# Performance work log

Measured on AMD Instinct MI355X. Metric: run time of the kernel, lower is better.

The kernel has to match this reference:

```python
import jax, jax.numpy as jnp
import numpy as np

# ---- static ragged feature layout (from CTGAN metadata) ----
NUM_CLUSTERS = [10, 8, 10, 5, 10, 10, 7, 10, 10, 10]          # per numerical feature
NUM_CATEGORIES = [2, 5, 10, 3, 50, 4, 2, 8, 100, 6, 2, 3, 12, 5, 2, 30, 4, 9, 2, 7]
TAU = 0.2        # GumbelSoftmax temperature (teras default)
BN_EPS = 1e-3    # keras BatchNormalization default epsilon
LATENT_DIM = 128
BATCH = 65536

_seg, _alpha = [], []
_gid = 0
for c in NUM_CLUSTERS:
    _seg.append(_gid); _alpha.append(True); _gid += 1        # alpha scalar (tanh), own segment
    _seg += [_gid] * c; _alpha += [False] * c; _gid += 1     # beta cluster group (gumbel softmax)
for k in NUM_CATEGORIES:
    _seg += [_gid] * k; _alpha += [False] * k; _gid += 1     # categorical group (gumbel softmax)
SEG = jnp.asarray(np.array(_seg, dtype=np.int32))
ALPHA_MASK = jnp.asarray(np.array(_alpha, dtype=bool))
N_SEG = _gid
DATA_DIM = len(_seg)  # 366


def setup_inputs() -> dict:
    key = jax.random.key(0)
    ks = jax.random.split(key, 8)
    z = jax.random.normal(ks[0], (BATCH, LATENT_DIM), dtype=jnp.float32)
    # pre-sampled standard Gumbel noise for the gumbel-softmax groups
    u = jax.random.uniform(ks[1], (BATCH, DATA_DIM), dtype=jnp.float32, minval=1e-6, maxval=1.0 - 1e-6)
    g = -jnp.log(-jnp.log(u))
    def w(k, fi, fo):
        return jax.random.normal(k, (fi, fo), dtype=jnp.float32) * (1.0 / np.sqrt(fi))
    return {
        "z": z, "g": g,
        "W1": w(ks[2], LATENT_DIM, 256), "b1": jnp.zeros((256,), jnp.float32),
        "gamma1": jnp.ones((256,), jnp.float32), "beta1": jnp.zeros((256,), jnp.float32),
        "W2": w(ks[3], LATENT_DIM + 256, 256), "b2": jnp.zeros((256,), jnp.float32),
        "gamma2": jnp.ones((256,), jnp.float32), "beta2": jnp.zeros((256,), jnp.float32),
        "Wout": w(ks[4], LATENT_DIM + 512, DATA_DIM), "bout": jnp.zeros((DATA_DIM,), jnp.float32),
    }


def _bn_relu(h, gamma, beta):
    # training-mode batch norm (batch statistics), as used while training CTGAN
    mu = jnp.mean(h, axis=0)
    var = jnp.var(h, axis=0)
    return jax.nn.relu((h - mu) * jax.lax.rsqrt(var + BN_EPS) * gamma + beta)


def reference(z, g, W1, b1, gamma1, beta1, W2, b2, gamma2, beta2, Wout, bout):
    # CTGAN residual generator layers: out = concat([relu(bn(dense(x))), x])
    h1 = jnp.concatenate([_bn_relu(z @ W1 + b1, gamma1, beta1), z], axis=1)    # [B, 384]
    h2 = jnp.concatenate([_bn_relu(h1 @ W2 + b2, gamma2, beta2), h1], axis=1)  # [B, 640]
    logits = h2 @ Wout + bout                                                  # [B, 366]

    # ragged per-group gumbel-softmax: segment-wise stable softmax over columns
    zt = ((logits + g) / TAU).T                                   # [D, B]
    m = jax.ops.segment_max(zt, SEG, num_segments=N_SEG)          # [S, B]
    e = jnp.exp(zt - m[SEG])
    s = jax.ops.segment_sum(e, SEG, num_segments=N_SEG)
    soft = (e / s[SEG]).T                                         # [B, D]
    # alpha columns: tanh of raw logits; all other columns: group softmax
    return jnp.where(ALPHA_MASK[None, :], jnp.tanh(logits), soft)
```

## Files before the change

kernel.cpp:

```cpp
#include <hip/hip_runtime.h>

typedef _Float16 half_t;
typedef _Float16 half4 __attribute__((ext_vector_type(4)));
typedef _Float16 half8 __attribute__((ext_vector_type(8)));
typedef float f32x4 __attribute__((ext_vector_type(4)));

#define AS1 __attribute__((address_space(1)))
#define AS3 __attribute__((address_space(3)))

static constexpr int NBATCH = 65536;

__device__ __forceinline__ bool is_alpha(int c) {
  const unsigned long long AM0 =
      (1ull << 0) | (1ull << 11) | (1ull << 20) | (1ull << 31) | (1ull << 37) |
      (1ull << 48) | (1ull << 59);
  const unsigned long long AM1 = (1ull << 3) | (1ull << 14) | (1ull << 25);
  if (c >= 90) return false;
  return (((c < 64) ? (AM0 >> c) : (AM1 >> (c - 64))) & 1ull) != 0ull;
}

__device__ __forceinline__ half8 bn8(half8 x, half8 sc, half8 sh, half8 lo) {
  return __builtin_elementwise_max(x * sc + sh, lo);
}

__global__ __launch_bounds__(256) void k_prep(
    const float* __restrict__ z, half_t* __restrict__ zdst,
    const float* __restrict__ W1, half_t* __restrict__ W1t,
    const float* __restrict__ W2, half_t* __restrict__ W2t,
    const float* __restrict__ Wout, half_t* __restrict__ Wot,
    half_t* __restrict__ t2sc, half_t* __restrict__ t2sh, half_t* __restrict__ t2lo,
    half_t* __restrict__ t3sc, half_t* __restrict__ t3sh, half_t* __restrict__ t3lo) {
  const int b = blockIdx.x;
  const int tid = threadIdx.x;
  if (b < 4096) {
    size_t i = (size_t)b * 256 + tid;
    int row = (int)(i >> 4), c8 = (int)(i & 15) << 3;
    const float* s = z + (size_t)row * 128 + c8;
    float4 v0 = *(const float4*)s;
    float4 v1 = *(const float4*)(s + 4);
    half8 h;
    h[0]=(half_t)v0.x; h[1]=(half_t)v0.y; h[2]=(half_t)v0.z; h[3]=(half_t)v0.w;
    h[4]=(half_t)v1.x; h[5]=(half_t)v1.y; h[6]=(half_t)v1.z; h[7]=(half_t)v1.w;
    *(half8*)(zdst + (size_t)row * 640 + c8) = h;
  } else if (b < 4224) {
    int i = (b - 4096) * 256 + tid;
    int n = i >> 7, k = i & 127;
    W1t[i] = (half_t)W1[k * 256 + n];
  } else if (b < 4608) {
    int i = (b - 4224) * 256 + tid;
    int n = i / 384, k = i - n * 384;
    W2t[i] = (half_t)W2[k * 256 + n];
  } else if (b < 5568) {
    int i = (b - 4608) * 256 + tid;
    int n = i / 640, k = i - n * 640;
    Wot[i] = (half_t)((n < 366) ? Wout[k * 366 + n] : 0.f);
  } else {
    if (tid < 128) {
      t2sc[256 + tid] = (half_t)1.f; t2sh[256 + tid] = (half_t)0.f;
      t2lo[256 + tid] = (half_t)(-65504.f);
    } else {
      int t = tid - 128;
      t3sc[512 + t] = (half_t)1.f; t3sh[512 + t] = (half_t)0.f;
      t3lo[512 + t] = (half_t)(-65504.f);
    }
  }
}

template<bool STATS, bool TRANS, bool ALPHA>
__global__ __launch_bounds__(256) void k_gemm(
    const half_t* __restrict__ A, int lda, int K,
    const half_t* __restrict__ Bt,
    const float* __restrict__ bias,
    const half_t* __restrict__ tsc, const half_t* __restrict__ tsh,
    const half_t* __restrict__ tlo,
    half_t* __restrict__ o16, int ldo, int ncreal,
    float* __restrict__ ps, float* __restrict__ pq) {
  __shared__ __align__(16) char smem[32768];
  const int tid  = threadIdx.x;
  const int lane = tid & 63;
  const int w    = tid >> 6;
  const int wr   = w >> 1, wc = w & 1;
  const int ml   = lane & 15, g = lane >> 4;
  const int brow = blockIdx.x * 128;
  const int bcol = blockIdx.y * 128;
  const int sr  = lane >> 3;
  const int scg = (lane & 7) ^ sr;

  f32x4 acc[4][4];
#pragma unroll
  for (int i = 0; i < 4; i++)
#pragma unroll
    for (int j = 0; j < 4; j++) acc[i][j] = (f32x4){0.f, 0.f, 0.f, 0.f};

  const half_t* Abase = A  + (size_t)brow * lda;
  const half_t* Bbase = Bt + (size_t)bcol * K;
  const int nt = K >> 6;

  half_t* As = (half_t*)smem;
  half_t* Bs = (half_t*)(smem + 16384);

  for (int t = 0; t < nt; t++) {
    const int k0 = t * 64;
    half8 sc0, sh0, lo0, sc1, sh1, lo1;
    if (TRANS) {
      const int ka = k0 + g * 8, kb = k0 + 32 + g * 8;
      sc0 = *(const half8*)&tsc[ka]; sh0 = *(const half8*)&tsh[ka]; lo0 = *(const half8*)&tlo[ka];
      sc1 = *(const half8*)&tsc[kb]; sh1 = *(const half8*)&tsh[kb]; lo1 = *(const half8*)&tlo[kb];
    }
    if (t) __syncthreads();
#pragma unroll
    for (int it = 0; it < 4; it++) {
      int q = it * 4 + w;
      int r = q * 8 + sr;
      __builtin_amdgcn_global_load_lds(
          (AS1 const void*)(Abase + (size_t)r * lda + k0 + scg * 8),
          (AS3 void*)(As + q * 512), 16, 0, 0);
      __builtin_amdgcn_global_load_lds(
          (AS1 const void*)(Bbase + (size_t)r * K + k0 + scg * 8),
          (AS3 void*)(Bs + q * 512), 16, 0, 0);
    }
    __syncthreads();
#pragma unroll
    for (int t2 = 0; t2 < 2; t2++) {
      const int c4 = t2 * 4 + g;
      half8 af[4], bf[4];
#pragma unroll
      for (int fm = 0; fm < 4; fm++) {
        int row = wr * 64 + fm * 16 + ml;
        af[fm] = *(const half8*)((const char*)As + row * 128 + ((c4 ^ (row & 7)) << 4));
      }
      if (TRANS) {
        const half8 sc = t2 ? sc1 : sc0;
        const half8 sh = t2 ? sh1 : sh0;
        const half8 lo = t2 ? lo1 : lo0;
#pragma unroll
        for (int fm = 0; fm < 4; fm++) af[fm] = bn8(af[fm], sc, sh, lo);
      }
#pragma unroll
      for (int fn = 0; fn < 4; fn++) {
        int row = wc * 64 + fn * 16 + ml;
        bf[fn] = *(const half8*)((const char*)Bs + row * 128 + ((c4 ^ (row & 7)) << 4));
      }
#pragma unroll
      for (int fm = 0; fm < 4; fm++)
#pragma unroll
        for (int fn = 0; fn < 4; fn++)
          acc[fm][fn] = __builtin_amdgcn_mfma_f32_16x16x32_f16(af[fm], bf[fn], acc[fm][fn], 0, 0, 0);
    }
  }
  __syncthreads();

#pragma unroll
  for (int fn = 0; fn < 4; fn++) {
    int col  = wc * 64 + fn * 16 + ml;
    int gcol = bcol + col;
    float bz = (gcol < ncreal) ? bias[gcol] : 0.f;
    float s = 0.f, q = 0.f;
    const bool al = ALPHA && (gcol < 90) && is_alpha(gcol);
#pragma unroll
    for (int fm = 0; fm < 4; fm++)
#pragma unroll
      for (int rr = 0; rr < 4; rr++) {
        float v = acc[fm][fn][rr] + bz;
        if (STATS) { s += v; q += v * v; }
        if (al) v = tanhf(v);
        acc[fm][fn][rr] = v;
      }
    if (STATS) {
      s += __shfl_xor(s, 16, 64); s += __shfl_xor(s, 32, 64);
      q += __shfl_xor(q, 16, 64); q += __shfl_xor(q, 32, 64);
      if (g == 0) {
        ps[(size_t)gcol * 1024 + blockIdx.x * 2 + wr] = s;
        pq[(size_t)gcol * 1024 + blockIdx.x * 2 + wr] = q;
      }
    }
  }

  half_t* so = (half_t*)smem;
#pragma unroll
  for (int fn = 0; fn < 4; fn++)
#pragma unroll
    for (int fm = 0; fm < 4; fm++)
#pragma unroll
      for (int rr = 0; rr < 4; rr++)
        so[(wr * 64 + fm * 16 + g * 4 + rr) * 128 + wc * 64 + fn * 16 + ml] =
            (half_t)acc[fm][fn][rr];
  __syncthreads();
#pragma unroll
  for (int it = 0; it < 8; it++) {
    int r = it * 16 + (tid >> 4);
    int c = (tid & 15) * 8;
    *(half8*)(o16 + (size_t)(brow + r) * ldo + bcol + c) = *(const half8*)&so[r * 128 + c];
  }
}

__global__ __launch_bounds__(256) void k_bnfinal(
    const float* __restrict__ ps, const float* __restrict__ pq,
    const float* __restrict__ gamma, const float* __restrict__ beta,
    half_t* __restrict__ scA, half_t* __restrict__ shA, half_t* __restrict__ loA,
    half_t* __restrict__ scB, half_t* __restrict__ shB, half_t* __restrict__ loB) {
  int c = blockIdx.x, t = threadIdx.x;
  float s = 0.f, q = 0.f;
#pragma unroll
  for (int i = 0; i < 4; i++) {
    s += ps[(size_t)c * 1024 + t + i * 256];
    q += pq[(size_t)c * 1024 + t + i * 256];
  }
#pragma unroll
  for (int o = 1; o < 64; o <<= 1) { s += __shfl_xor(s, o, 64); q += __shfl_xor(q, o, 64); }
  __shared__ float ss[4], qq[4];
  if ((t & 63) == 0) { ss[t >> 6] = s; qq[t >> 6] = q; }
  __syncthreads();
  if (t == 0) {
    s = ss[0] + ss[1] + ss[2] + ss[3];
    q = qq[0] + qq[1] + qq[2] + qq[3];
    float mu   = s * (1.f / NBATCH);
    float var  = fmaxf(q * (1.f / NBATCH) - mu * mu, 0.f);
    float rstd = rsqrtf(var + 1e-3f);
    float a  = gamma[c] * rstd;
    float sh = beta[c] - mu * a;
    scA[c] = (half_t)a; shA[c] = (half_t)sh; loA[c] = (half_t)0.f;
    if (scB) { scB[c] = (half_t)a; shB[c] = (half_t)sh; loB[c] = (half_t)0.f; }
  }
}

template<int L>
__device__ __forceinline__ void seg_norm(float* __restrict__ zr, int S, int Lr) {
  float v[L];
#pragma unroll
  for (int j = 0; j < L; j++) v[j] = (j < Lr) ? zr[S + j] : -1e30f;
  float m = -1e30f;
#pragma unroll
  for (int j = 0; j < L; j++) m = fmaxf(m, v[j]);
  float s = 0.f;
#pragma unroll
  for (int j = 0; j < L; j++) { float e = __expf(v[j] - m); v[j] = e; s += e; }
  const float inv = 1.0f / s;
#pragma unroll
  for (int j = 0; j < L; j++)
    if (j < Lr) zr[S + j] = v[j] * inv;
}

template<int H>
__device__ __forceinline__ void seg_quad(float* __restrict__ zr, int base, int n) {
  float v[H];
#pragma unroll
  for (int j = 0; j < H; j++) v[j] = (j < n) ? zr[base + j] : -1e30f;
  float m = -1e30f;
#pragma unroll
  for (int j = 0; j < H; j++) m = fmaxf(m, v[j]);
  m = fmaxf(m, __shfl_xor(m, 1, 64));
  m = fmaxf(m, __shfl_xor(m, 2, 64));
  float s = 0.f;
#pragma unroll
  for (int j = 0; j < H; j++) { float e = __expf(v[j] - m); v[j] = e; s += e; }
  s += __shfl_xor(s, 1, 64);
  s += __shfl_xor(s, 2, 64);
  const float inv = 1.0f / s;
#pragma unroll
  for (int j = 0; j < H; j++)
    if (j < n) zr[base + j] = v[j] * inv;
}

__global__ __launch_bounds__(256, 6) void k_softmax(const half_t* __restrict__ lg,
                                                    const float* __restrict__ g,
                                                    float* __restrict__ out) {
  __shared__ float zb[16][373];
  const int tid  = threadIdx.x;
  const int row0 = blockIdx.x * 16;
  const size_t gbase = (size_t)row0 * 366;
  for (int i2 = tid; i2 < 16 * 183; i2 += 256) {
    int e0 = i2 * 2;
    int r = e0 / 366;
    int c = e0 - r * 366;
    const half_t* lp = lg + (size_t)(row0 + r) * 384 + c;
    float lx = (float)lp[0], ly = (float)lp[1];
    float2 gg = *(const float2*)(g + gbase + e0);
    zb[r][c]     = is_alpha(c)     ? lx : (lx + gg.x) * 5.0f;
    zb[r][c + 1] = is_alpha(c + 1) ? ly : (ly + gg.y) * 5.0f;
  }
  __syncthreads();
  {
    const int lane = tid & 63;
    const int w    = tid >> 6;
    const int quad = lane & 3;
    float* zr = &zb[lane >> 2][0];
    switch (w) {
      case 0:
        seg_quad<25>(zr, 184 + quad * 25, 25);
        break;
      case 1:
        seg_quad<13>(zr, 120 + quad * 13 - (quad >> 1) * (quad & 1), 13 - (quad >> 1));
        seg_quad<8>(zr, 314 + quad * 8 - (quad >> 1) * (quad & 1), 8 - (quad >> 1));
        break;
      case 2: {
        int s0 = (quad == 0) ? 295 : (quad == 1) ? 107 : (quad == 2) ? 38 : 68;
        int l0 = (quad == 0) ? 12 : 10;
        int s1 = (quad == 0) ? 1 : (quad == 1) ? 21 : (quad == 2) ? 49 : 79;
        int s2 = (quad == 0) ? 0 : (quad == 1) ? 100 : (quad == 2) ? 174 : 290;
        int l2 = (quad == 0) ? 0 : 2;
        seg_norm<12>(zr, s0, l0);
        seg_norm<10>(zr, s1, 10);
        seg_norm<2>(zr, s2, l2);
        break;
      }
      default: {
        int s0 = (quad == 0) ? 90 : (quad == 1) ? 12 : (quad == 2) ? 60 : 102;
        int l0 = (quad == 0) ? 10 : (quad == 1) ? 8 : (quad == 2) ? 7 : 5;
        int s1 = (quad == 0) ? 348 : (quad == 1) ? 176 : (quad == 2) ? 359 : 307;
        int l1 = (quad == 0) ? 9 : (quad == 1) ? 8 : (quad == 2) ? 7 : 5;
        int s2 = (quad == 0) ? 312 : (quad == 1) ? 284 : (quad == 2) ? 32 : 170;
        int l2 = (quad == 0) ? 2 : (quad == 1) ? 6 : (quad == 2) ? 5 : 4;
        int s3 = (quad == 0) ? 117 : (quad == 1) ? 357 : (quad == 2) ? 292 : 344;
        int l3 = (quad == 0) ? 3 : (quad == 1) ? 2 : (quad == 2) ? 3 : 4;
        seg_norm<10>(zr, s0, l0);
        seg_norm<9>(zr, s1, l1);
        seg_norm<6>(zr, s2, l2);
        seg_norm<4>(zr, s3, l3);
        break;
      }
    }
  }
  __syncthreads();
  for (int i2 = tid; i2 < 16 * 183; i2 += 256) {
    int e0 = i2 * 2;
    int r = e0 / 366;
    int c = e0 - r * 366;
    float2 v;
    v.x = zb[r][c];
    v.y = zb[r][c + 1];
    *(float2*)(out + gbase + e0) = v;
  }
}

extern "C" void kernel_launch(void* const* d_in, const int* in_sizes, int n_in,
                              void* d_out, int out_size, void* d_ws, size_t ws_size,
                              hipStream_t stream) {
  const float* z      = (const float*)d_in[0];
  const float* g      = (const float*)d_in[1];
  const float* W1     = (const float*)d_in[2];
  const float* b1     = (const float*)d_in[3];
  const float* gamma1 = (const float*)d_in[4];
  const float* beta1  = (const float*)d_in[5];
  const float* W2     = (const float*)d_in[6];
  const float* b2     = (const float*)d_in[7];
  const float* gamma2 = (const float*)d_in[8];
  const float* beta2  = (const float*)d_in[9];
  const float* Wout   = (const float*)d_in[10];
  const float* bout   = (const float*)d_in[11];
  float* out = (float*)d_out;
  char* ws = (char*)d_ws;

  size_t off = 0;
  half_t* act = (half_t*)(ws + off); off += (size_t)NBATCH * 640 * 2;
  half_t* lg  = (half_t*)(ws + off); off += (size_t)NBATCH * 384 * 2;
  half_t* W1t = (half_t*)(ws + off); off += (size_t)256 * 128 * 2;
  half_t* W2t = (half_t*)(ws + off); off += (size_t)256 * 384 * 2;
  half_t* Wot = (half_t*)(ws + off); off += (size_t)384 * 640 * 2;
  float*  ps  = (float*)(ws + off);  off += (size_t)256 * 1024 * 4;
  float*  pq  = (float*)(ws + off);  off += (size_t)256 * 1024 * 4;
  half_t* t2sc = (half_t*)(ws + off); off += 1024;
  half_t* t2sh = (half_t*)(ws + off); off += 1024;
  half_t* t2lo = (half_t*)(ws + off); off += 1024;
  half_t* t3sc = (half_t*)(ws + off); off += 2048;
  half_t* t3sh = (half_t*)(ws + off); off += 2048;
  half_t* t3lo = (half_t*)(ws + off); off += 2048;
  (void)ws_size; (void)in_sizes; (void)n_in; (void)out_size;

  k_prep<<<5569, 256, 0, stream>>>(z, act + 512, W1, W1t, W2, W2t, Wout, Wot,
                                   t2sc, t2sh, t2lo, t3sc, t3sh, t3lo);

  k_gemm<true, false, false><<<dim3(512, 2), 256, 0, stream>>>(
      act + 512, 640, 128, W1t, b1, nullptr, nullptr, nullptr,
      act + 256, 640, 256, ps, pq);
  k_bnfinal<<<256, 256, 0, stream>>>(ps, pq, gamma1, beta1,
                                     t2sc, t2sh, t2lo, t3sc + 256, t3sh + 256, t3lo + 256);

  k_gemm<true, true, false><<<dim3(512, 2), 256, 0, stream>>>(
      act + 256, 640, 384, W2t, b2, t2sc, t2sh, t2lo,
      act + 0, 640, 256, ps, pq);
  k_bnfinal<<<256, 256, 0, stream>>>(ps, pq, gamma2, beta2,
                                     t3sc, t3sh, t3lo, nullptr, nullptr, nullptr);

  k_gemm<false, true, true><<<dim3(512, 3), 256, 0, stream>>>(
      act, 640, 640, Wot, bout, t3sc, t3sh, t3lo,
      lg, 384, 366, nullptr, nullptr);

  k_softmax<<<NBATCH / 16, 256, 0, stream>>>(lg, g, out);
}
```

Baseline: 176.3 us.

## Triple-buffer GEMM K-loop with async global-to-LDS prefetch two tiles ahead

The GEMM main loop moves from a single-buffered 64-wide K tile, with two barriers per tile, to a 32-wide K tile held in a three-stage LDS ring. Loads for tile t+2 are issued before computing tile t, and raw s_waitcnt vmcnt plus a single s_barrier per step replace the double sync. The batch-norm scale, shift and clamp vectors are staged into LDS once at kernel start instead of being read from global memory every tile. In exchange, LDS use grows to 52 KB, which may reduce the number of resident blocks, and correctness depends on the hand-chosen vmcnt counts.

Result: no change. 178.1 us (+1.0%).

```diff
diff --git a/kernel.cpp b/kernel.cpp
--- a/kernel.cpp
+++ b/kernel.cpp
@@ -75,7 +75,7 @@
     const half_t* __restrict__ tlo,
     half_t* __restrict__ o16, int ldo, int ncreal,
     float* __restrict__ ps, float* __restrict__ pq) {
-  __shared__ __align__(16) char smem[32768];
+  __shared__ __align__(16) char smem[53248];
   const int tid  = threadIdx.x;
   const int lane = tid & 63;
   const int w    = tid >> 6;
@@ -83,8 +83,6 @@
   const int ml   = lane & 15, g = lane >> 4;
   const int brow = blockIdx.x * 128;
   const int bcol = blockIdx.y * 128;
-  const int sr  = lane >> 3;
-  const int scg = (lane & 7) ^ sr;
 
   f32x4 acc[4][4];
 #pragma unroll
@@ -94,60 +92,80 @@
 
   const half_t* Abase = A  + (size_t)brow * lda;
   const half_t* Bbase = Bt + (size_t)bcol * K;
-  const int nt = K >> 6;
-
-  half_t* As = (half_t*)smem;
-  half_t* Bs = (half_t*)(smem + 16384);
-
-  for (int t = 0; t < nt; t++) {
-    const int k0 = t * 64;
-    half8 sc0, sh0, lo0, sc1, sh1, lo1;
+  const int nt = K >> 5;
+
+  auto stage = [&](int t, int p) {
+    const int k0 = t * 32;
+    char* dst = smem + p * 16384;
+#pragma unroll
+    for (int it = 0; it < 2; it++) {
+      int cb = it * 256 + w * 64;
+      int ch = cb + lane;
+      int row = ch >> 2;
+      int sc2 = (ch & 3) ^ (row & 3);
+      __builtin_amdgcn_global_load_lds(
+          (AS1 const void*)(Abase + (size_t)row * lda + k0 + sc2 * 8),
+          (AS3 void*)(dst + cb * 16), 16, 0, 0);
+      __builtin_amdgcn_global_load_lds(
+          (AS1 const void*)(Bbase + (size_t)row * K + k0 + sc2 * 8),
+          (AS3 void*)(dst + 8192 + cb * 16), 16, 0, 0);
+    }
+  };
+
+  auto compute = [&](int t, int p) {
+    const char* As = smem + p * 16384;
+    const char* Bs = As + 8192;
+    half8 sc, sh, lo;
     if (TRANS) {
-      const int ka = k0 + g * 8, kb = k0 + 32 + g * 8;
-      sc0 = *(const half8*)&tsc[ka]; sh0 = *(const half8*)&tsh[ka]; lo0 = *(const half8*)&tlo[ka];
-      sc1 = *(const half8*)&tsc[kb]; sh1 = *(const half8*)&tsh[kb]; lo1 = *(const half8*)&tlo[kb];
-    }
-    if (t) __syncthreads();
-#pragma unroll
-    for (int it = 0; it < 4; it++) {
-      int q = it * 4 + w;
-      int r = q * 8 + sr;
-      __builtin_amdgcn_global_load_lds(
-          (AS1 const void*)(Abase + (size_t)r * lda + k0 + scg * 8),
-          (AS3 void*)(As + q * 512), 16, 0, 0);
-      __builtin_amdgcn_global_load_lds(
-          (AS1 const void*)(Bbase + (size_t)r * K + k0 + scg * 8),
-          (AS3 void*)(Bs + q * 512), 16, 0, 0);
-    }
-    __syncthreads();
-#pragma unroll
-    for (int t2 = 0; t2 < 2; t2++) {
-      const int c4 = t2 * 4 + g;
-      half8 af[4], bf[4];
-#pragma unroll
-      for (int fm = 0; fm < 4; fm++) {
-        int row = wr * 64 + fm * 16 + ml;
-        af[fm] = *(const half8*)((const char*)As + row * 128 + ((c4 ^ (row & 7)) << 4));
-      }
-      if (TRANS) {
-        const half8 sc = t2 ? sc1 : sc0;
-        const half8 sh = t2 ? sh1 : sh0;
-        const half8 lo = t2 ? lo1 : lo0;
-#pragma unroll
-        for (int fm = 0; fm < 4; fm++) af[fm] = bn8(af[fm], sc, sh, lo);
-      }
-#pragma unroll
-      for (int fn = 0; fn < 4; fn++) {
-        int row = wc * 64 + fn * 16 + ml;
-        bf[fn] = *(const half8*)((const char*)Bs + row * 128 + ((c4 ^ (row & 7)) << 4));
-      }
-#pragma unroll
-      for (int fm = 0; fm < 4; fm++)
-#pragma unroll
-        for (int fn = 0; fn < 4; fn++)
-          acc[fm][fn] = __builtin_amdgcn_mfma_f32_16x16x32_f16(af[fm], bf[fn], acc[fm][fn], 0, 0, 0);
-    }
-  }
+      const half_t* tb = (const half_t*)(smem + 49152);
+      int o = (t * 4 + g) * 8;
+      sc = *(const half8*)(tb + o);
+      sh = *(const half8*)(tb + 640 + o);
+      lo = *(const half8*)(tb + 1280 + o);
+    }
+    half8 af[4], bf[4];
+#pragma unroll
+    for (int fm = 0; fm < 4; fm++) {
+      int row = wr * 64 + fm * 16 + ml;
+      af[fm] = *(const half8*)(As + row * 64 + ((g ^ (row & 3)) << 4));
+    }
+    if (TRANS) {
+#pragma unroll
+      for (int fm = 0; fm < 4; fm++) af[fm] = bn8(af[fm], sc, sh, lo);
+    }
+#pragma unroll
+    for (int fn = 0; fn < 4; fn++) {
+      int row = wc * 64 + fn * 16 + ml;
+      bf[fn] = *(const half8*)(Bs + row * 64 + ((g ^ (row & 3)) << 4));
+    }
+#pragma unroll
+    for (int fm = 0; fm < 4; fm++)
+#pragma unroll
+      for (int fn = 0; fn < 4; fn++)
+        acc[fm][fn] = __builtin_amdgcn_mfma_f32_16x16x32_f16(af[fm], bf[fn], acc[fm][fn], 0, 0, 0);
+  };
+
+  if (TRANS) {
+    const int no = K >> 3;
+    for (int i = tid; i < 3 * no; i += 256) {
+      int a = i / no, pos = i - a * no;
+      const half_t* src = (a == 0 ? tsc : (a == 1 ? tsh : tlo)) + pos * 8;
+      *(half8*)(smem + 49152 + a * 1280 + pos * 16) = *(const half8*)src;
+    }
+  }
+  stage(0, 0);
+  stage(1, 1);
+  asm volatile("s_waitcnt lgkmcnt(0)" ::: "memory");
+
+  for (int t = 0; t < nt - 1; t++) {
+    asm volatile("s_waitcnt vmcnt(4)" ::: "memory");
+    __builtin_amdgcn_s_barrier();
+    if (t + 2 < nt) stage(t + 2, (t + 2) % 3);
+    compute(t, t % 3);
+  }
+  asm volatile("s_waitcnt vmcnt(0)" ::: "memory");
+  __builtin_amdgcn_s_barrier();
+  compute(nt - 1, (nt - 1) % 3);
   __syncthreads();
 
 #pragma unroll
```
